# Kernel optimization log

Measured on AMD Instinct MI355X. Metric: run time of the kernel, lower is better.

Reference implementation:

```python
import jax, jax.numpy as jnp
import numpy as np

D_MODEL = 384
D_INNER = 768          # expand * d_model
NHEADS = 12            # d_inner // headdim
HEADDIM = 64
DSTATE = 64
CONV_DIM = D_INNER + 2 * DSTATE       # 896
D_IN_PROJ = 2 * D_INNER + 2 * DSTATE + NHEADS  # 1676
LN_EPS = 1e-5


def _avg_pool_3x3(x):
    # 3x3 avg pool, stride 1, SAME padding, count_include_pad=False
    sums = jax.lax.reduce_window(x, 0.0, jax.lax.add, (1, 1, 3, 3), (1, 1, 1, 1), 'SAME')
    ones = jnp.ones((1, 1) + x.shape[2:], x.dtype)
    cnt = jax.lax.reduce_window(ones, 0.0, jax.lax.add, (1, 1, 3, 3), (1, 1, 1, 1), 'SAME')
    return sums / cnt


def setup_inputs() -> dict:
    key = jax.random.key(0)
    ks = jax.random.split(key, 8)
    B, H, W = 8, 56, 56
    L = H * W
    # dt_bias init as in the torch module
    dt = jnp.exp(jax.random.uniform(ks[5], (NHEADS,)) * (np.log(0.1) - np.log(0.001)) + np.log(0.001))
    dt = jnp.clip(dt, 1e-4, None)
    dt_bias = dt + jnp.log(-jnp.expm1(-dt))
    A_log = jnp.log(jax.random.uniform(ks[6], (D_INNER,), minval=1.0, maxval=16.0))
    return {
        'x': jax.random.normal(ks[0], (B, L, D_MODEL), jnp.float32),
        'in_proj_w': jax.random.normal(ks[1], (D_IN_PROJ, D_MODEL), jnp.float32) * 0.05,
        'conv_w': jax.random.normal(ks[2], (CONV_DIM, 1, 3, 3), jnp.float32) * 0.1,
        'conv_b': jnp.zeros((CONV_DIM,), jnp.float32),
        'dt_bias': dt_bias,
        'A_log': A_log,
        'D': jnp.ones((NHEADS,), jnp.float32),
        'norm_w': jnp.ones((D_INNER,), jnp.float32),
        'norm_b': jnp.zeros((D_INNER,), jnp.float32),
        'out_proj_w': jax.random.normal(ks[3], (D_MODEL, D_INNER), jnp.float32) * 0.05,
        'H': H,
        'W': W,
    }


def reference(x, in_proj_w, conv_w, conv_b, dt_bias, A_log, D, norm_w, norm_b, out_proj_w, H, W):
    B, L, _ = x.shape
    # in_proj and split: z | xBC | dt
    zxbcdt = x @ in_proj_w.T                                   # (B, L, 1676)
    z = zxbcdt[..., :D_INNER]                                   # (B, L, 768)
    xBC = zxbcdt[..., D_INNER:D_INNER + CONV_DIM]               # (B, L, 896)
    dt = jax.nn.softplus(zxbcdt[..., D_INNER + CONV_DIM:] + dt_bias)  # (B, L, 12)
    # depthwise 3x3 conv over the HxW grid + SiLU
    xBC_img = xBC.reshape(B, H, W, CONV_DIM).transpose(0, 3, 1, 2)
    xBC_img = jax.lax.conv_general_dilated(
        xBC_img, conv_w, (1, 1), 'SAME', feature_group_count=CONV_DIM)
    xBC_img = xBC_img + conv_b[None, :, None, None]
    xBC = jax.nn.silu(xBC_img).transpose(0, 2, 3, 1).reshape(B, L, CONV_DIM)
    xs = xBC[..., :D_INNER].reshape(B, L, NHEADS, HEADDIM)
    Bm = xBC[..., D_INNER:D_INNER + DSTATE]                     # (B, L, dstate)
    Cm = xBC[..., D_INNER + DSTATE:]                            # (B, L, dstate)
    # ssm_op (ngroups == 1, pattern == 'LoDSA')
    A = -jnp.exp(A_log).reshape(NHEADS, HEADDIM)                # (h, d)
    x_in = xs.transpose(0, 2, 1, 3)                             # (B, h, L, d)
    dA = dt.transpose(0, 2, 1)[..., None] * A[None, :, None, :] # (B, h, L, d)
    dx = dA * x_in                                              # (B, h, L, d)
    # (B,h,L,d) -> (B,h,H,W,d) -> (B, h*d, H, W), pool, back
    dx_img = dx.reshape(B, NHEADS, H, W, HEADDIM).transpose(0, 1, 4, 2, 3)
    dx_img = dx_img.reshape(B, NHEADS * HEADDIM, H, W)
    dx_pool = _avg_pool_3x3(dx_img)
    dx = dx_pool.reshape(B, NHEADS, HEADDIM, L).transpose(0, 1, 3, 2)  # (B, h, L, d)
    # linear-attention style global aggregation (replaces the scan)
    h_state = jnp.einsum('bls,bhld->bhsd', Bm, dx)              # (B, h, s, d)
    Ch = jnp.einsum('bls,bhsd->bhld', Cm, h_state)              # (B, h, L, d)
    y = Ch + x_in * D[None, :, None, None]
    y = y.transpose(0, 2, 1, 3).reshape(B, L, D_INNER)
    # gated layernorm + out projection
    g = y * jax.nn.silu(z)
    mu = g.mean(-1, keepdims=True)
    var = ((g - mu) ** 2).mean(-1, keepdims=True)
    gn = (g - mu) / jnp.sqrt(var + LN_EPS) * norm_w + norm_b
    return gn @ out_proj_w.T
```

## Files before the change

kernel.cpp:

```cpp
#include <hip/hip_runtime.h>
#include <hip/hip_bf16.h>
#include <math.h>

#define BB 8
#define HH 56
#define WW 56
#define LL (HH*WW)
#define DMODEL 384
#define DINNER 768
#define NH 12
#define HD 64
#define DS 64
#define CDIM (DINNER + 2*DS)
#define NPROJ (2*DINNER + 2*DS + NH)
#define NPAD 1792
#define MTOT (BB*LL)
#define LN_EPS 1e-5f
#define NCG (CDIM/8)
#define NDG (DINNER/8)
#define SPLITL 7

typedef __attribute__((ext_vector_type(8))) _Float16 f16x8;
typedef __attribute__((ext_vector_type(4))) float f32x4;

__device__ __forceinline__ ushort f2hu(float v) {
    union { _Float16 h; ushort u; } cv; cv.h = (_Float16)v; return cv.u;
}
__device__ __forceinline__ float hu2f(ushort u) {
    union { ushort u; _Float16 h; } cv; cv.u = u; return (float)cv.h;
}

__global__ __launch_bounds__(256) void k_cast_x(
    const float4* __restrict__ in, ushort4* __restrict__ out)
{
    int i = blockIdx.x * 256 + threadIdx.x;
    float4 v = in[i];
    ushort4 h;
    h.x = f2hu(v.x); h.y = f2hu(v.y); h.z = f2hu(v.z); h.w = f2hu(v.w);
    out[i] = h;
}

__global__ __launch_bounds__(256) void k_cast_w1(
    const float* __restrict__ w, ushort4* __restrict__ out)
{
    int i = blockIdx.x * 256 + threadIdx.x;
    int n = i / (DMODEL / 4);
    int k = (i % (DMODEL / 4)) * 4;
    ushort4 h = {0,0,0,0};
    if (n < NPROJ) {
        float4 v = *(const float4*)(w + (size_t)n * DMODEL + k);
        h.x = f2hu(v.x); h.y = f2hu(v.y); h.z = f2hu(v.z); h.w = f2hu(v.w);
    }
    out[i] = h;
}

__global__ __launch_bounds__(256) void k_cast_w2(
    const float4* __restrict__ in, ushort4* __restrict__ out)
{
    int i = blockIdx.x * 256 + threadIdx.x;
    float4 v = in[i];
    ushort4 h;
    h.x = f2hu(v.x); h.y = f2hu(v.y); h.z = f2hu(v.z); h.w = f2hu(v.w);
    out[i] = h;
}

#define LDSW 40
__global__ __launch_bounds__(256) void k_gemm1_mfma(
    const ushort* __restrict__ xh, const ushort* __restrict__ wh,
    const float* __restrict__ dt_bias,
    ushort* __restrict__ zbuf, ushort* __restrict__ xbcbuf, float* __restrict__ dtbuf)
{
    __shared__ ushort As[128 * LDSW];
    __shared__ ushort Bs[128 * LDSW];
    const int m0 = blockIdx.y * 128;
    const int n0 = blockIdx.x * 128;
    const int tid = threadIdx.x;
    const int wid = tid >> 6;
    const int lane = tid & 63;
    const int r = lane & 15;
    const int quad = lane >> 4;
    const int wm = (wid >> 1) * 64;
    const int wn = (wid & 1) * 64;
    const int srow = tid >> 2;
    const int scol = (tid & 3) * 8;

    f32x4 acc[4][4];
#pragma unroll
    for (int i = 0; i < 4; ++i)
#pragma unroll
        for (int j = 0; j < 4; ++j) acc[i][j] = (f32x4){0.f, 0.f, 0.f, 0.f};

    for (int k0 = 0; k0 < DMODEL; k0 += 32) {
        int4 a0 = *(const int4*)(xh + (size_t)(m0 + srow)      * DMODEL + k0 + scol);
        int4 a1 = *(const int4*)(xh + (size_t)(m0 + srow + 64) * DMODEL + k0 + scol);
        int4 b0 = *(const int4*)(wh + (size_t)(n0 + srow)      * DMODEL + k0 + scol);
        int4 b1 = *(const int4*)(wh + (size_t)(n0 + srow + 64) * DMODEL + k0 + scol);
        __syncthreads();
        *(int4*)(As + srow * LDSW + scol)        = a0;
        *(int4*)(As + (srow + 64) * LDSW + scol) = a1;
        *(int4*)(Bs + srow * LDSW + scol)        = b0;
        *(int4*)(Bs + (srow + 64) * LDSW + scol) = b1;
        __syncthreads();
        f16x8 af[4], bfr[4];
#pragma unroll
        for (int t = 0; t < 4; ++t) {
            af[t]  = *(const f16x8*)(As + (wm + t * 16 + r) * LDSW + quad * 8);
            bfr[t] = *(const f16x8*)(Bs + (wn + t * 16 + r) * LDSW + quad * 8);
        }
#pragma unroll
        for (int i = 0; i < 4; ++i)
#pragma unroll
            for (int j = 0; j < 4; ++j)
                acc[i][j] = __builtin_amdgcn_mfma_f32_16x16x32_f16(af[i], bfr[j], acc[i][j], 0, 0, 0);
    }
#pragma unroll
    for (int i = 0; i < 4; ++i) {
#pragma unroll
        for (int j = 0; j < 4; ++j) {
            int n = n0 + wn + j * 16 + r;
            if (n >= NPROJ) continue;
#pragma unroll
            for (int v = 0; v < 4; ++v) {
                int m = m0 + wm + i * 16 + quad * 4 + v;
                float val = acc[i][j][v];
                if (n < DINNER) {
                    zbuf[(size_t)m * DINNER + n] = f2hu(val);
                } else if (n < DINNER + CDIM) {
                    xbcbuf[(size_t)m * CDIM + (n - DINNER)] = f2hu(val);
                } else {
                    int h = n - (DINNER + CDIM);
                    float t = val + dt_bias[h];
                    float sp = (t > 20.f) ? t : log1pf(expf(t));
                    dtbuf[(size_t)m * NH + h] = sp;
                }
            }
        }
    }
}

__global__ __launch_bounds__(256) void k_gemm2_mfma(
    const ushort* __restrict__ gn, const ushort* __restrict__ wh,
    float* __restrict__ out)
{
    __shared__ ushort As[128 * LDSW];
    __shared__ ushort Bs[128 * LDSW];
    const int m0 = blockIdx.y * 128;
    const int n0 = blockIdx.x * 128;
    const int tid = threadIdx.x;
    const int wid = tid >> 6;
    const int lane = tid & 63;
    const int r = lane & 15;
    const int quad = lane >> 4;
    const int wm = (wid >> 1) * 64;
    const int wn = (wid & 1) * 64;
    const int srow = tid >> 2;
    const int scol = (tid & 3) * 8;

    f32x4 acc[4][4];
#pragma unroll
    for (int i = 0; i < 4; ++i)
#pragma unroll
        for (int j = 0; j < 4; ++j) acc[i][j] = (f32x4){0.f, 0.f, 0.f, 0.f};

    for (int k0 = 0; k0 < DINNER; k0 += 32) {
        int4 a0 = *(const int4*)(gn + (size_t)(m0 + srow)      * DINNER + k0 + scol);
        int4 a1 = *(const int4*)(gn + (size_t)(m0 + srow + 64) * DINNER + k0 + scol);
        int4 b0 = *(const int4*)(wh + (size_t)(n0 + srow)      * DINNER + k0 + scol);
        int4 b1 = *(const int4*)(wh + (size_t)(n0 + srow + 64) * DINNER + k0 + scol);
        __syncthreads();
        *(int4*)(As + srow * LDSW + scol)        = a0;
        *(int4*)(As + (srow + 64) * LDSW + scol) = a1;
        *(int4*)(Bs + srow * LDSW + scol)        = b0;
        *(int4*)(Bs + (srow + 64) * LDSW + scol) = b1;
        __syncthreads();
        f16x8 af[4], bfr[4];
#pragma unroll
        for (int t = 0; t < 4; ++t) {
            af[t]  = *(const f16x8*)(As + (wm + t * 16 + r) * LDSW + quad * 8);
            bfr[t] = *(const f16x8*)(Bs + (wn + t * 16 + r) * LDSW + quad * 8);
        }
#pragma unroll
        for (int i = 0; i < 4; ++i)
#pragma unroll
            for (int j = 0; j < 4; ++j)
                acc[i][j] = __builtin_amdgcn_mfma_f32_16x16x32_f16(af[i], bfr[j], acc[i][j], 0, 0, 0);
    }
#pragma unroll
    for (int i = 0; i < 4; ++i) {
#pragma unroll
        for (int j = 0; j < 4; ++j) {
            int n = n0 + wn + j * 16 + r;
#pragma unroll
            for (int v = 0; v < 4; ++v) {
                int m = m0 + wm + i * 16 + quad * 4 + v;
                out[(size_t)m * DMODEL + n] = acc[i][j][v];
            }
        }
    }
}

__global__ __launch_bounds__(256) void k_conv(
    const ushort* __restrict__ xbc, const float* __restrict__ cw,
    const float* __restrict__ cb, ushort* __restrict__ out)
{
    const int gid = blockIdx.x * 256 + threadIdx.x;
    const int cg  = gid % NCG;
    const int pix = gid / NCG;
    const int b = pix / LL, ij = pix % LL;
    const int i = ij / WW, j = ij % WW;
    const int c0 = cg * 8;

    float wreg[72];
#pragma unroll
    for (int t = 0; t < 18; ++t)
        *(float4*)(wreg + t * 4) = *(const float4*)(cw + c0 * 9 + t * 4);
    float acc[8];
    {
        float4 b0 = *(const float4*)(cb + c0);
        float4 b1 = *(const float4*)(cb + c0 + 4);
        acc[0]=b0.x; acc[1]=b0.y; acc[2]=b0.z; acc[3]=b0.w;
        acc[4]=b1.x; acc[5]=b1.y; acc[6]=b1.z; acc[7]=b1.w;
    }
#pragma unroll
    for (int ky = 0; ky < 3; ++ky) {
        int ii = i + ky - 1;
        if (ii < 0 || ii >= HH) continue;
#pragma unroll
        for (int kx = 0; kx < 3; ++kx) {
            int jj = j + kx - 1;
            if (jj < 0 || jj >= WW) continue;
            union { int4 q; ushort u[8]; } xv;
            xv.q = *(const int4*)(xbc + ((size_t)b * LL + ii * WW + jj) * CDIM + c0);
            int t = ky * 3 + kx;
#pragma unroll
            for (int q = 0; q < 8; ++q)
                acc[q] += wreg[q * 9 + t] * hu2f(xv.u[q]);
        }
    }
    union { int4 q; ushort u[8]; } o;
#pragma unroll
    for (int q = 0; q < 8; ++q) {
        float s = acc[q] / (1.f + expf(-acc[q]));
        o.u[q] = f2hu(s);
    }
    *(int4*)(out + (size_t)pix * CDIM + c0) = o.q;
}

__global__ __launch_bounds__(256) void k_dxpool(
    const ushort* __restrict__ xbc_conv, const float* __restrict__ dtbuf,
    const float* __restrict__ A_log, ushort* __restrict__ dxp)
{
    const int gid = blockIdx.x * 256 + threadIdx.x;
    const int cg  = gid % NDG;
    const int pix = gid / NDG;
    const int b = pix / LL, l = pix % LL;
    const int i = l / WW, j = l % WW;
    const int c0 = cg * 8;
    const int h = c0 >> 6;

    float Ah[8];
    {
        float4 a0 = *(const float4*)(A_log + c0);
        float4 a1 = *(const float4*)(A_log + c0 + 4);
        Ah[0]=a0.x; Ah[1]=a0.y; Ah[2]=a0.z; Ah[3]=a0.w;
        Ah[4]=a1.x; Ah[5]=a1.y; Ah[6]=a1.z; Ah[7]=a1.w;
    }
#pragma unroll
    for (int q = 0; q < 8; ++q) Ah[q] = -expf(Ah[q]);

    float sum[8] = {0.f,0.f,0.f,0.f,0.f,0.f,0.f,0.f};
    int cnt = 0;
#pragma unroll
    for (int dy = -1; dy <= 1; ++dy) {
        int ii = i + dy;
        if (ii < 0 || ii >= HH) continue;
#pragma unroll
        for (int dxx = -1; dxx <= 1; ++dxx) {
            int jj = j + dxx;
            if (jj < 0 || jj >= WW) continue;
            int ll = ii * WW + jj;
            ++cnt;
            float dtv = dtbuf[((size_t)b * LL + ll) * NH + h];
            union { int4 q; ushort u[8]; } xv;
            xv.q = *(const int4*)(xbc_conv + ((size_t)b * LL + ll) * CDIM + c0);
#pragma unroll
            for (int q = 0; q < 8; ++q)
                sum[q] += dtv * hu2f(xv.u[q]);
        }
    }
    float inv = 1.f / (float)cnt;
    union { int4 q; ushort u[8]; } o;
#pragma unroll
    for (int q = 0; q < 8; ++q)
        o.u[q] = f2hu(Ah[q] * sum[q] * inv);
    *(int4*)(dxp + (((size_t)b * NH + h) * LL + l) * HD + (c0 & 63)) = o.q;
}

#define LDSP 33
__global__ __launch_bounds__(256) void k_hstate_mfma(
    const ushort* __restrict__ xbc_conv, const ushort* __restrict__ dxp,
    float* __restrict__ hpart)
{
    __shared__ ushort DsT[64 * LDSP];
    __shared__ ushort BsT[64 * LDSP];
    const int lc = blockIdx.x;
    const int bh = blockIdx.y;
    const int b = bh / NH;
    const int tid = threadIdx.x;
    const int wid = tid >> 6;
    const int lane = tid & 63;
    const int r = lane & 15;
    const int quad = lane >> 4;
    const int wd = (wid >> 1) * 32;
    const int wsn = (wid & 1) * 32;
    const int lt = tid >> 3;
    const int sg = (tid & 7) * 8;

    f32x4 acc[2][2];
#pragma unroll
    for (int i = 0; i < 2; ++i)
#pragma unroll
        for (int j = 0; j < 2; ++j) acc[i][j] = (f32x4){0.f, 0.f, 0.f, 0.f};

    const int l_base = lc * (LL / SPLITL);
    for (int step = 0; step < (LL / SPLITL) / 32; ++step) {
        int l0 = l_base + step * 32;
        union { int4 q; ushort u[8]; } dv, bv;
        dv.q = *(const int4*)(dxp + (((size_t)bh) * LL + l0 + lt) * HD + sg);
        bv.q = *(const int4*)(xbc_conv + ((size_t)(b * LL + l0 + lt)) * CDIM + DINNER + sg);
        __syncthreads();
#pragma unroll
        for (int q = 0; q < 8; ++q) {
            DsT[(sg + q) * LDSP + lt] = dv.u[q];
            BsT[(sg + q) * LDSP + lt] = bv.u[q];
        }
        __syncthreads();
        f16x8 af[2], bf[2];
#pragma unroll
        for (int t = 0; t < 2; ++t) {
            af[t] = *(const f16x8*)(DsT + (wd + t * 16 + r) * LDSP + quad * 8);
            bf[t] = *(const f16x8*)(BsT + (wsn + t * 16 + r) * LDSP + quad * 8);
        }
#pragma unroll
        for (int i = 0; i < 2; ++i)
#pragma unroll
            for (int j = 0; j < 2; ++j)
                acc[i][j] = __builtin_amdgcn_mfma_f32_16x16x32_f16(af[i], bf[j], acc[i][j], 0, 0, 0);
    }
    float* outp = hpart + ((size_t)(lc * 96 + bh) << 12);
#pragma unroll
    for (int i = 0; i < 2; ++i)
#pragma unroll
        for (int j = 0; j < 2; ++j)
#pragma unroll
            for (int v = 0; v < 4; ++v)
                outp[(wd + i * 16 + quad * 4 + v) * 64 + (wsn + j * 16 + r)] = acc[i][j][v];
}

__global__ __launch_bounds__(256) void k_hprep(
    const float* __restrict__ hpart, ushort* __restrict__ hT)
{
    int i = blockIdx.x * 256 + threadIdx.x;
    int bh = i >> 12;
    int rem = i & 4095;
    float v = 0.f;
#pragma unroll
    for (int lc = 0; lc < SPLITL; ++lc)
        v += hpart[((size_t)(lc * 96 + bh) << 12) + rem];
    hT[i] = f2hu(v);
}

#define HTW 72
__global__ __launch_bounds__(256) void k_chy_mfma(
    const ushort* __restrict__ xbc_conv, const ushort* __restrict__ hT,
    const float* __restrict__ Dp, ushort* __restrict__ ybuf)
{
    __shared__ ushort Hs[64 * HTW];
    const int bh = blockIdx.y;
    const int b = bh / NH, h = bh % NH;
    const int tid = threadIdx.x;
    const int wid = tid >> 6;
    const int lane = tid & 63;
    const int r = lane & 15;
    const int quad = lane >> 4;

    for (int idx = tid; idx < 512; idx += 256) {
        int row = idx >> 3, c8 = (idx & 7) * 8;
        *(int4*)(Hs + row * HTW + c8) = *(const int4*)(hT + ((size_t)bh << 12) + row * 64 + c8);
    }
    __syncthreads();

    const int chunk = blockIdx.x * 4 + wid;
    if (chunk >= 49) return;
    const int l0 = chunk * 64;

    f32x4 acc[4][4];
#pragma unroll
    for (int i = 0; i < 4; ++i)
#pragma unroll
        for (int j = 0; j < 4; ++j) acc[i][j] = (f32x4){0.f, 0.f, 0.f, 0.f};

#pragma unroll
    for (int kk = 0; kk < 2; ++kk) {
        f16x8 af[4], bfr[4];
#pragma unroll
        for (int t = 0; t < 4; ++t) {
            af[t] = *(const f16x8*)(xbc_conv +
                ((size_t)(b * LL + l0 + t * 16 + r)) * CDIM + DINNER + DS + kk * 32 + quad * 8);
            bfr[t] = *(const f16x8*)(Hs + (t * 16 + r) * HTW + kk * 32 + quad * 8);
        }
#pragma unroll
        for (int i = 0; i < 4; ++i)
#pragma unroll
            for (int j = 0; j < 4; ++j)
                acc[i][j] = __builtin_amdgcn_mfma_f32_16x16x32_f16(af[i], bfr[j], acc[i][j], 0, 0, 0);
    }
    const float Dh = Dp[h];
#pragma unroll
    for (int i = 0; i < 4; ++i) {
#pragma unroll
        for (int j = 0; j < 4; ++j) {
            int d = j * 16 + r;
#pragma unroll
            for (int v = 0; v < 4; ++v) {
                int l = l0 + i * 16 + quad * 4 + v;
                float xv = hu2f(xbc_conv[((size_t)(b * LL + l)) * CDIM + h * HD + d]);
                ybuf[((size_t)(b * LL + l)) * DINNER + h * HD + d] = f2hu(acc[i][j][v] + xv * Dh);
            }
        }
    }
}

__global__ __launch_bounds__(256) void k_gln(
    const ushort* __restrict__ ybuf, const ushort* __restrict__ zbuf,
    const float* __restrict__ nw, const float* __restrict__ nb,
    ushort* __restrict__ gnbuf)
{
    const int row = blockIdx.x * 4 + (threadIdx.x >> 6);
    const int lane = threadIdx.x & 63;
    const size_t base = (size_t)row * DINNER;

    float g[12];
    float sum = 0.f, sumsq = 0.f;
#pragma unroll
    for (int p = 0; p < 3; ++p) {
        int c = lane * 4 + p * 256;
        union { ushort4 q; ushort u[4]; } yv, zv;
        yv.q = *(const ushort4*)(ybuf + base + c);
        zv.q = *(const ushort4*)(zbuf + base + c);
#pragma unroll
        for (int q = 0; q < 4; ++q) {
            float y = hu2f(yv.u[q]);
            float z = hu2f(zv.u[q]);
            float gv = y * (z / (1.f + expf(-z)));
            g[p * 4 + q] = gv;
            sum += gv;
            sumsq += gv * gv;
        }
    }
#pragma unroll
    for (int off = 32; off > 0; off >>= 1) {
        sum += __shfl_xor(sum, off, 64);
        sumsq += __shfl_xor(sumsq, off, 64);
    }
    const float mu = sum / (float)DINNER;
    const float var = sumsq / (float)DINNER - mu * mu;
    const float rstd = rsqrtf(var + LN_EPS);
#pragma unroll
    for (int p = 0; p < 3; ++p) {
        int c = lane * 4 + p * 256;
        float4 w = *(const float4*)(nw + c);
        float4 bb = *(const float4*)(nb + c);
        union { ushort4 q; ushort u[4]; } o;
        o.u[0] = f2hu((g[p*4+0] - mu) * rstd * w.x + bb.x);
        o.u[1] = f2hu((g[p*4+1] - mu) * rstd * w.y + bb.y);
        o.u[2] = f2hu((g[p*4+2] - mu) * rstd * w.z + bb.z);
        o.u[3] = f2hu((g[p*4+3] - mu) * rstd * w.w + bb.w);
        *(ushort4*)(gnbuf + base + c) = o.q;
    }
}

extern "C" void kernel_launch(void* const* d_in, const int* in_sizes, int n_in,
                              void* d_out, int out_size, void* d_ws, size_t ws_size,
                              hipStream_t stream)
{
    const float* x         = (const float*)d_in[0];
    const float* in_proj_w = (const float*)d_in[1];
    const float* conv_w    = (const float*)d_in[2];
    const float* conv_b    = (const float*)d_in[3];
    const float* dt_bias   = (const float*)d_in[4];
    const float* A_log     = (const float*)d_in[5];
    const float* Dp        = (const float*)d_in[6];
    const float* norm_w    = (const float*)d_in[7];
    const float* norm_b    = (const float*)d_in[8];
    const float* out_proj_w= (const float*)d_in[9];

    char* wsb = (char*)d_ws;
    float*  dtbuf   = (float*) (wsb + 0);
    ushort* w1      = (ushort*)(wsb + 2777088);
    ushort* w2      = (ushort*)(wsb + 4153344);
    ushort* zbuf    = (ushort*)(wsb + 4743168);
    ushort* xbcraw  = (ushort*)(wsb + 43278336);
    ushort* xbcconv = (ushort*)(wsb + 88236032);
    ushort* x16     = xbcconv;
    ushort* hT      = xbcraw;
    float*  hpart   = (float*)(wsb + 44851200);
    ushort* dxp     = (ushort*)d_out;
    ushort* ybuf    = (ushort*)d_out;
    ushort* gnbuf   = xbcraw;

    k_cast_x <<<MTOT * DMODEL / 4 / 256, 256, 0, stream>>>(
        (const float4*)x, (ushort4*)x16);
    k_cast_w1<<<NPAD * DMODEL / 4 / 256, 256, 0, stream>>>(
        in_proj_w, (ushort4*)w1);
    k_cast_w2<<<DMODEL * DINNER / 4 / 256, 256, 0, stream>>>(
        (const float4*)out_proj_w, (ushort4*)w2);

    k_gemm1_mfma<<<dim3(NPAD / 128, MTOT / 128), 256, 0, stream>>>(
        x16, w1, dt_bias, zbuf, xbcraw, dtbuf);

    k_conv<<<MTOT * NCG / 256, 256, 0, stream>>>(
        xbcraw, conv_w, conv_b, xbcconv);
    k_dxpool<<<MTOT * NDG / 256, 256, 0, stream>>>(
        xbcconv, dtbuf, A_log, dxp);
    k_hstate_mfma<<<dim3(SPLITL, BB * NH), 256, 0, stream>>>(
        xbcconv, dxp, hpart);
    k_hprep<<<96 * 4096 / 256, 256, 0, stream>>>(hpart, hT);
    k_chy_mfma<<<dim3(13, BB * NH), 256, 0, stream>>>(
        xbcconv, hT, Dp, ybuf);
    k_gln<<<MTOT / 4, 256, 0, stream>>>(
        ybuf, zbuf, norm_w, norm_b, gnbuf);
    k_gemm2_mfma<<<dim3(DMODEL / 128, MTOT / 128), 256, 0, stream>>>(
        gnbuf, w2, (float*)d_out);
}
```

Measured before the change: 425.4 us.

## Double-buffer LDS tiles in both projection GEMMs and merge weight cast kernels

Both MFMA GEMMs now use two LDS buffers: the next K-tile is loaded from global memory into registers before the current tile's MFMAs run, then written to the alternate buffer, so only one barrier per iteration remains instead of two. The two weight-cast kernels are merged into one launch to cut launch overhead. LDS use per block doubles, which could lower occupancy, and register pressure rises from holding the prefetched tiles.

```diff
diff --git a/kernel.cpp b/kernel.cpp
--- a/kernel.cpp
+++ b/kernel.cpp
@@ -40,28 +40,29 @@
     out[i] = h;
 }
 
-__global__ __launch_bounds__(256) void k_cast_w1(
-    const float* __restrict__ w, ushort4* __restrict__ out)
+#define W1Q (NPAD*DMODEL/4)
+#define W2Q (DMODEL*DINNER/4)
+__global__ __launch_bounds__(256) void k_cast_w(
+    const float* __restrict__ w1src, const float* __restrict__ w2src,
+    ushort4* __restrict__ w1dst, ushort4* __restrict__ w2dst)
 {
     int i = blockIdx.x * 256 + threadIdx.x;
-    int n = i / (DMODEL / 4);
-    int k = (i % (DMODEL / 4)) * 4;
-    ushort4 h = {0,0,0,0};
-    if (n < NPROJ) {
-        float4 v = *(const float4*)(w + (size_t)n * DMODEL + k);
+    if (i < W1Q) {
+        int n = i / (DMODEL / 4);
+        int k = (i % (DMODEL / 4)) * 4;
+        ushort4 h = {0,0,0,0};
+        if (n < NPROJ) {
+            float4 v = *(const float4*)(w1src + (size_t)n * DMODEL + k);
+            h.x = f2hu(v.x); h.y = f2hu(v.y); h.z = f2hu(v.z); h.w = f2hu(v.w);
+        }
+        w1dst[i] = h;
+    } else {
+        int t = i - W1Q;
+        float4 v = ((const float4*)w2src)[t];
+        ushort4 h;
         h.x = f2hu(v.x); h.y = f2hu(v.y); h.z = f2hu(v.z); h.w = f2hu(v.w);
-    }
-    out[i] = h;
-}
-
-__global__ __launch_bounds__(256) void k_cast_w2(
-    const float4* __restrict__ in, ushort4* __restrict__ out)
-{
-    int i = blockIdx.x * 256 + threadIdx.x;
-    float4 v = in[i];
-    ushort4 h;
-    h.x = f2hu(v.x); h.y = f2hu(v.y); h.z = f2hu(v.z); h.w = f2hu(v.w);
-    out[i] = h;
+        w2dst[t] = h;
+    }
 }
 
 #define LDSW 40
@@ -70,8 +71,8 @@
     const float* __restrict__ dt_bias,
     ushort* __restrict__ zbuf, ushort* __restrict__ xbcbuf, float* __restrict__ dtbuf)
 {
-    __shared__ ushort As[128 * LDSW];
-    __shared__ ushort Bs[128 * LDSW];
+    __shared__ ushort As[2][128 * LDSW];
+    __shared__ ushort Bs[2][128 * LDSW];
     const int m0 = blockIdx.y * 128;
     const int n0 = blockIdx.x * 128;
     const int tid = threadIdx.x;
@@ -90,28 +91,47 @@
 #pragma unroll
         for (int j = 0; j < 4; ++j) acc[i][j] = (f32x4){0.f, 0.f, 0.f, 0.f};
 
-    for (int k0 = 0; k0 < DMODEL; k0 += 32) {
-        int4 a0 = *(const int4*)(xh + (size_t)(m0 + srow)      * DMODEL + k0 + scol);
-        int4 a1 = *(const int4*)(xh + (size_t)(m0 + srow + 64) * DMODEL + k0 + scol);
-        int4 b0 = *(const int4*)(wh + (size_t)(n0 + srow)      * DMODEL + k0 + scol);
-        int4 b1 = *(const int4*)(wh + (size_t)(n0 + srow + 64) * DMODEL + k0 + scol);
-        __syncthreads();
-        *(int4*)(As + srow * LDSW + scol)        = a0;
-        *(int4*)(As + (srow + 64) * LDSW + scol) = a1;
-        *(int4*)(Bs + srow * LDSW + scol)        = b0;
-        *(int4*)(Bs + (srow + 64) * LDSW + scol) = b1;
-        __syncthreads();
+    {
+        int4 a0 = *(const int4*)(xh + (size_t)(m0 + srow)      * DMODEL + scol);
+        int4 a1 = *(const int4*)(xh + (size_t)(m0 + srow + 64) * DMODEL + scol);
+        int4 b0 = *(const int4*)(wh + (size_t)(n0 + srow)      * DMODEL + scol);
+        int4 b1 = *(const int4*)(wh + (size_t)(n0 + srow + 64) * DMODEL + scol);
+        *(int4*)(As[0] + srow * LDSW + scol)        = a0;
+        *(int4*)(As[0] + (srow + 64) * LDSW + scol) = a1;
+        *(int4*)(Bs[0] + srow * LDSW + scol)        = b0;
+        *(int4*)(Bs[0] + (srow + 64) * LDSW + scol) = b1;
+    }
+    __syncthreads();
+
+    int cur = 0;
+    for (int k0 = 32; k0 <= DMODEL; k0 += 32) {
+        const bool has = (k0 < DMODEL);
+        int4 na0, na1, nb0, nb1;
+        if (has) {
+            na0 = *(const int4*)(xh + (size_t)(m0 + srow)      * DMODEL + k0 + scol);
+            na1 = *(const int4*)(xh + (size_t)(m0 + srow + 64) * DMODEL + k0 + scol);
+            nb0 = *(const int4*)(wh + (size_t)(n0 + srow)      * DMODEL + k0 + scol);
+            nb1 = *(const int4*)(wh + (size_t)(n0 + srow + 64) * DMODEL + k0 + scol);
+        }
         f16x8 af[4], bfr[4];
 #pragma unroll
         for (int t = 0; t < 4; ++t) {
-            af[t]  = *(const f16x8*)(As + (wm + t * 16 + r) * LDSW + quad * 8);
-            bfr[t] = *(const f16x8*)(Bs + (wn + t * 16 + r) * LDSW + quad * 8);
+            af[t]  = *(const f16x8*)(As[cur] + (wm + t * 16 + r) * LDSW + quad * 8);
+            bfr[t] = *(const f16x8*)(Bs[cur] + (wn + t * 16 + r) * LDSW + quad * 8);
         }
 #pragma unroll
         for (int i = 0; i < 4; ++i)
 #pragma unroll
             for (int j = 0; j < 4; ++j)
                 acc[i][j] = __builtin_amdgcn_mfma_f32_16x16x32_f16(af[i], bfr[j], acc[i][j], 0, 0, 0);
+        if (has) {
+            *(int4*)(As[cur ^ 1] + srow * LDSW + scol)        = na0;
+            *(int4*)(As[cur ^ 1] + (srow + 64) * LDSW + scol) = na1;
+            *(int4*)(Bs[cur ^ 1] + srow * LDSW + scol)        = nb0;
+            *(int4*)(Bs[cur ^ 1] + (srow + 64) * LDSW + scol) = nb1;
+            __syncthreads();
+            cur ^= 1;
+        }
     }
 #pragma unroll
     for (int i = 0; i < 4; ++i) {
@@ -142,8 +162,8 @@
     const ushort* __restrict__ gn, const ushort* __restrict__ wh,
     float* __restrict__ out)
 {
-    __shared__ ushort As[128 * LDSW];
-    __shared__ ushort Bs[128 * LDSW];
+    __shared__ ushort As[2][128 * LDSW];
+    __shared__ ushort Bs[2][128 * LDSW];
     const int m0 = blockIdx.y * 128;
     const int n0 = blockIdx.x * 128;
     const int tid = threadIdx.x;
@@ -162,28 +182,47 @@
 #pragma unroll
         for (int j = 0; j < 4; ++j) acc[i][j] = (f32x4){0.f, 0.f, 0.f, 0.f};
 
-    for (int k0 = 0; k0 < DINNER; k0 += 32) {
-        int4 a0 = *(const int4*)(gn + (size_t)(m0 + srow)      * DINNER + k0 + scol);
-        int4 a1 = *(const int4*)(gn + (size_t)(m0 + srow + 64) * DINNER + k0 + scol);
-        int4 b0 = *(const int4*)(wh + (size_t)(n0 + srow)      * DINNER + k0 + scol);
-        int4 b1 = *(const int4*)(wh + (size_t)(n0 + srow + 64) * DINNER + k0 + scol);
-        __syncthreads();
-        *(int4*)(As + srow * LDSW + scol)        = a0;
-        *(int4*)(As + (srow + 64) * LDSW + scol) = a1;
-        *(int4*)(Bs + srow * LDSW + scol)        = b0;
-        *(int4*)(Bs + (srow + 64) * LDSW + scol) = b1;
-        __syncthreads();
+    {
+        int4 a0 = *(const int4*)(gn + (size_t)(m0 + srow)      * DINNER + scol);
+        int4 a1 = *(const int4*)(gn + (size_t)(m0 + srow + 64) * DINNER + scol);
+        int4 b0 = *(const int4*)(wh + (size_t)(n0 + srow)      * DINNER + scol);
+        int4 b1 = *(const int4*)(wh + (size_t)(n0 + srow + 64) * DINNER + scol);
+        *(int4*)(As[0] + srow * LDSW + scol)        = a0;
+        *(int4*)(As[0] + (srow + 64) * LDSW + scol) = a1;
+        *(int4*)(Bs[0] + srow * LDSW + scol)        = b0;
+        *(int4*)(Bs[0] + (srow + 64) * LDSW + scol) = b1;
+    }
+    __syncthreads();
+
+    int cur = 0;
+    for (int k0 = 32; k0 <= DINNER; k0 += 32) {
+        const bool has = (k0 < DINNER);
+        int4 na0, na1, nb0, nb1;
+        if (has) {
+            na0 = *(const int4*)(gn + (size_t)(m0 + srow)      * DINNER + k0 + scol);
+            na1 = *(const int4*)(gn + (size_t)(m0 + srow + 64) * DINNER + k0 + scol);
+            nb0 = *(const int4*)(wh + (size_t)(n0 + srow)      * DINNER + k0 + scol);
+            nb1 = *(const int4*)(wh + (size_t)(n0 + srow + 64) * DINNER + k0 + scol);
+        }
         f16x8 af[4], bfr[4];
 #pragma unroll
         for (int t = 0; t < 4; ++t) {
-            af[t]  = *(const f16x8*)(As + (wm + t * 16 + r) * LDSW + quad * 8);
-            bfr[t] = *(const f16x8*)(Bs + (wn + t * 16 + r) * LDSW + quad * 8);
+            af[t]  = *(const f16x8*)(As[cur] + (wm + t * 16 + r) * LDSW + quad * 8);
+            bfr[t] = *(const f16x8*)(Bs[cur] + (wn + t * 16 + r) * LDSW + quad * 8);
         }
 #pragma unroll
         for (int i = 0; i < 4; ++i)
 #pragma unroll
             for (int j = 0; j < 4; ++j)
                 acc[i][j] = __builtin_amdgcn_mfma_f32_16x16x32_f16(af[i], bfr[j], acc[i][j], 0, 0, 0);
+        if (has) {
+            *(int4*)(As[cur ^ 1] + srow * LDSW + scol)        = na0;
+            *(int4*)(As[cur ^ 1] + (srow + 64) * LDSW + scol) = na1;
+            *(int4*)(Bs[cur ^ 1] + srow * LDSW + scol)        = nb0;
+            *(int4*)(Bs[cur ^ 1] + (srow + 64) * LDSW + scol) = nb1;
+            __syncthreads();
+            cur ^= 1;
+        }
     }
 #pragma unroll
     for (int i = 0; i < 4; ++i) {
@@ -511,10 +550,8 @@
 
     k_cast_x <<<MTOT * DMODEL / 4 / 256, 256, 0, stream>>>(
         (const float4*)x, (ushort4*)x16);
-    k_cast_w1<<<NPAD * DMODEL / 4 / 256, 256, 0, stream>>>(
-        in_proj_w, (ushort4*)w1);
-    k_cast_w2<<<DMODEL * DINNER / 4 / 256, 256, 0, stream>>>(
-        (const float4*)out_proj_w, (ushort4*)w2);
+    k_cast_w<<<(W1Q + W2Q) / 256, 256, 0, stream>>>(
+        in_proj_w, out_proj_w, (ushort4*)w1, (ushort4*)w2);
 
     k_gemm1_mfma<<<dim3(NPAD / 128, MTOT / 128), 256, 0, stream>>>(
         x16, w1, dt_bias, zbuf, xbcraw, dtbuf);
```

Result: faster. 411.8 us (-3.2%).
